# Optimization experiments

Hardware: AMD Instinct MI355X
Metric: run time of the kernel (lower is better)

## Reference

```python
import jax, jax.numpy as jnp
import numpy as np

B, T, P, C = 32, 16, 16, 2048
EPS = 1e-5


def setup_inputs() -> dict:
    key = jax.random.key(0)
    ks = jax.random.split(key, 9)
    s = 0.02
    return {
        "X": jax.random.normal(ks[0], (B, T, P, C), dtype=jnp.float32),
        "W_att": jax.random.normal(ks[1], (C, C), dtype=jnp.float32) * s,
        "b_att": jnp.zeros((C,), dtype=jnp.float32),
        "W1": jax.random.normal(ks[2], (C, C), dtype=jnp.float32) * s,
        "b1": jnp.zeros((C,), dtype=jnp.float32),
        "gamma": jnp.ones((C,), dtype=jnp.float32),
        "beta": jnp.zeros((C,), dtype=jnp.float32),
        "W2": jax.random.normal(ks[3], (C, C), dtype=jnp.float32) * s,
        "b2": jnp.zeros((C,), dtype=jnp.float32),
    }


def reference(X, W_att, b_att, W1, b1, gamma, beta, W2, b2):
    b, t, p, c = X.shape
    Xf = X.reshape(b * t, p, c)                                   # [BT, P, C]
    # per-frame attention gate: mean over parts -> Linear -> sigmoid
    attn = jax.nn.sigmoid(jnp.einsum("nc,dc->nd", Xf.mean(axis=1), W_att) + b_att)
    Xg = Xf * attn[:, None, :]                                    # gate each part
    # gcn: Linear -> per-frame BatchNorm1d (training stats over P) -> ReLU -> Linear
    h = jnp.einsum("npc,dc->npd", Xg, W1) + b1                    # [BT, P, C]
    mu = h.mean(axis=1, keepdims=True)
    var = jnp.mean(jnp.square(h - mu), axis=1, keepdims=True)     # biased var, as torch BN
    hn = (h - mu) * jax.lax.rsqrt(var + EPS) * gamma + beta
    out = jnp.einsum("npc,dc->npd", jax.nn.relu(hn), W2) + b2
    return out.reshape(b, t, p, c)
```

## Files before the change

kernel.cpp:

```cpp
#include <hip/hip_runtime.h>
#include <hip/hip_bf16.h>

typedef __attribute__((ext_vector_type(8))) short short8;
typedef __attribute__((ext_vector_type(4))) float f32x4;

static constexpr int Cdim = 2048;
static constexpr int NFRM = 512;
static constexpr int Pdim = 16;
static constexpr int MROWS = NFRM * Pdim;
static constexpr float EPS = 1e-5f;

__device__ __forceinline__ unsigned short f2b(float x) {
  union { float f; unsigned u; } v; v.f = x;
  unsigned r = v.u + 0x7fffu + ((v.u >> 16) & 1u);
  return (unsigned short)(r >> 16);
}

__device__ __forceinline__ void gload16(const void* g, void* l) {
  __builtin_amdgcn_global_load_lds(
      (const __attribute__((address_space(1))) unsigned int*)g,
      (__attribute__((address_space(3))) unsigned int*)l, 16, 0, 0);
}


__global__ __launch_bounds__(256) void cast3_kernel(
    const float* __restrict__ s0, const float* __restrict__ s1, const float* __restrict__ s2,
    unsigned short* __restrict__ d0, unsigned short* __restrict__ d1, unsigned short* __restrict__ d2)
{
  long i = (long)blockIdx.x * 256 + threadIdx.x;
  const float* s; unsigned short* d; long off;
  if (i < 1048576)      { s = s0; d = d0; off = i; }
  else if (i < 2097152) { s = s1; d = d1; off = i - 1048576; }
  else                  { s = s2; d = d2; off = i - 2097152; }
  float4 v = reinterpret_cast<const float4*>(s)[off];
  union { unsigned short u[4]; unsigned long long q; } o;
  o.u[0] = f2b(v.x); o.u[1] = f2b(v.y); o.u[2] = f2b(v.z); o.u[3] = f2b(v.w);
  *reinterpret_cast<unsigned long long*>(d + off * 4) = o.q;
}

__global__ __launch_bounds__(256) void mean_cast_kernel(
    const float* __restrict__ X, unsigned short* __restrict__ Mb)
{
  int idx = blockIdx.x * 256 + threadIdx.x;
  int n  = idx >> 9;
  int c4 = idx & 511;
  const float4* xp = reinterpret_cast<const float4*>(X) + (long)n * (Pdim * 512) + c4;
  float4 s = {0.f, 0.f, 0.f, 0.f};
  #pragma unroll
  for (int p = 0; p < Pdim; ++p) {
    float4 v = xp[(long)p * 512];
    s.x += v.x; s.y += v.y; s.z += v.z; s.w += v.w;
  }
  const float r = 1.f / 16.f;
  union { unsigned short u[4]; unsigned long long q; } o;
  o.u[0] = f2b(s.x * r); o.u[1] = f2b(s.y * r); o.u[2] = f2b(s.z * r); o.u[3] = f2b(s.w * r);
  *reinterpret_cast<unsigned long long*>(Mb + (long)idx * 4) = o.q;
}

__global__ __launch_bounds__(256) void gate_kernel(
    const float* __restrict__ X, const float* __restrict__ PA, const float* __restrict__ PB,
    const float* __restrict__ b_att, unsigned short* __restrict__ Xg)
{
  constexpr long F = 512L * 2048;
  long idx = (long)blockIdx.x * 256 + threadIdx.x;
  int c4 = (int)(idx & 511);
  long np = idx >> 9;
  long n  = np >> 4;
  float4 x  = reinterpret_cast<const float4*>(X)[idx];
  float4 p0 = reinterpret_cast<const float4*>(PA)[n * 512 + c4];
  float4 p1 = reinterpret_cast<const float4*>(PA + F)[n * 512 + c4];
  float4 p2 = reinterpret_cast<const float4*>(PB)[n * 512 + c4];
  float4 p3 = reinterpret_cast<const float4*>(PB + F)[n * 512 + c4];
  float4 bb = reinterpret_cast<const float4*>(b_att)[c4];
  float4 a;
  a.x = 1.f / (1.f + __expf(-(p0.x + p1.x + p2.x + p3.x + bb.x)));
  a.y = 1.f / (1.f + __expf(-(p0.y + p1.y + p2.y + p3.y + bb.y)));
  a.z = 1.f / (1.f + __expf(-(p0.z + p1.z + p2.z + p3.z + bb.z)));
  a.w = 1.f / (1.f + __expf(-(p0.w + p1.w + p2.w + p3.w + bb.w)));
  union { unsigned short u[4]; unsigned long long q; } o;
  o.u[0] = f2b(x.x * a.x); o.u[1] = f2b(x.y * a.y);
  o.u[2] = f2b(x.z * a.z); o.u[3] = f2b(x.w * a.w);
  *reinterpret_cast<unsigned long long*>(Xg + idx * 4) = o.q;
}

__global__ __launch_bounds__(256) void gemm_att_sk(
    const unsigned short* __restrict__ A,
    const unsigned short* __restrict__ B,
    float* __restrict__ PA, float* __restrict__ PB)
{
  constexpr int N = 2048, K = 2048, KH = 512;
  constexpr long F = 512L * 2048;
  __shared__ unsigned short As[128 * 32];
  __shared__ unsigned short Bs[128 * 32];
  const int t = threadIdx.x;
  const int lane = t & 63;
  const int wid = t >> 6;
  const int wr = wid >> 1, wc = wid & 1;
  const int m0 = blockIdx.x * 128, n0 = blockIdx.y * 128;
  const int k0 = blockIdx.z * KH;
  float* out = (blockIdx.z < 2) ? (PA + (long)blockIdx.z * F) : (PB + (long)(blockIdx.z - 2) * F);

  f32x4 acc[4][4];
  #pragma unroll
  for (int i = 0; i < 4; i++)
    #pragma unroll
    for (int j = 0; j < 4; j++) acc[i][j] = (f32x4){0.f, 0.f, 0.f, 0.f};

  const int srow = t >> 2;
  const int scol = (t & 3) * 8;
  const long aoff0 = (long)(m0 + srow) * K + scol;
  const long aoff1 = (long)(m0 + 64 + srow) * K + scol;
  const long boff0 = (long)(n0 + srow) * K + scol;
  const long boff1 = (long)(n0 + 64 + srow) * K + scol;
  char* AsB = (char*)As;
  char* BsB = (char*)Bs;

  const int fr = lane & 15;
  const int fk = (lane >> 4) * 8;

  for (int kt = k0; kt < k0 + KH; kt += 32) {
    __syncthreads();
    gload16(A + aoff0 + kt, AsB + t * 16);
    gload16(A + aoff1 + kt, AsB + 4096 + t * 16);
    gload16(B + boff0 + kt, BsB + t * 16);
    gload16(B + boff1 + kt, BsB + 4096 + t * 16);
    __syncthreads();
    short8 af[4], bfr[4];
    #pragma unroll
    for (int m = 0; m < 4; m++)
      af[m] = *reinterpret_cast<const short8*>(&As[(wr * 64 + m * 16 + fr) * 32 + fk]);
    #pragma unroll
    for (int n = 0; n < 4; n++)
      bfr[n] = *reinterpret_cast<const short8*>(&Bs[(wc * 64 + n * 16 + fr) * 32 + fk]);
    #pragma unroll
    for (int m = 0; m < 4; m++)
      #pragma unroll
      for (int n = 0; n < 4; n++)
        acc[m][n] = __builtin_amdgcn_mfma_f32_16x16x32_bf16(af[m], bfr[n], acc[m][n], 0, 0, 0);
  }

  const int l4 = lane >> 4;
  #pragma unroll
  for (int m = 0; m < 4; m++) {
    const int r0 = m0 + wr * 64 + m * 16 + l4 * 4;
    #pragma unroll
    for (int n = 0; n < 4; n++) {
      const int cn = n0 + wc * 64 + n * 16 + fr;
      #pragma unroll
      for (int j = 0; j < 4; j++)
        out[(long)(r0 + j) * N + cn] = acc[m][n][j];
    }
  }
}

template<int EPI>
__global__ __launch_bounds__(512, 2) void gemm256(
    const unsigned short* __restrict__ A,
    const unsigned short* __restrict__ Bp,
    int Kk, int Nn, int nbx,
    const float* __restrict__ bias,
    const float* __restrict__ gamma,
    const float* __restrict__ beta,
    float* __restrict__ Cf,
    unsigned short* __restrict__ Cb)
{
  __shared__ char lds[131072];
  const int t = threadIdx.x;
  const int lane = t & 63;
  const int wid = t >> 6;
  const int wr = wid >> 2;
  const int wc = wid & 3;

  const int nw = gridDim.x;
  const int wg = (blockIdx.x & 7) * (nw >> 3) + (blockIdx.x >> 3);
  const int bx = wg % nbx;
  const int by = wg / nbx;
  const int m0 = bx << 8, n0 = by << 8;

  const int NT = Kk >> 6;
  const int NI = NT >> 1;

  const long h64 = (long)64 * Kk, h128 = (long)128 * Kk;
  const int row0 = t >> 3;
  const int col0 = ((t & 7) * 8) ^ ((row0 & 7) << 3);
  const unsigned short* gA = A  + (long)(m0 + row0) * Kk + col0;
  const unsigned short* gB = Bp + (long)(n0 + row0) * Kk + col0;

  const int fr_ = lane & 15;
  const int cb0 = ((lane >> 4) << 4) ^ ((fr_ & 7) << 4);
  const int aB = (wr << 14) + fr_ * 128;
  const int bB = 32768 + ((wc >> 1) << 14) + ((wc & 1) << 13) + fr_ * 128;

#define STG(gp_, ko_, lo_) do { \
    const unsigned short* g0_ = (gp_) + (ko_); \
    gload16(g0_, lds + (lo_) + (t << 4)); \
    gload16(g0_ + h64, lds + (lo_) + 8192 + (t << 4)); } while (0)

#define LDSA(buf_, m_, ks_) (*(const short8*)(lds + (buf_) * 65536 + aB + (m_) * 2048 + (cb0 ^ ((ks_) << 6))))
#define LDSB(buf_, n_, ks_) (*(const short8*)(lds + (buf_) * 65536 + bB + (n_) * 2048 + (cb0 ^ ((ks_) << 6))))

#define RDAF(buf_, mb_) do { \
    af[0][0] = LDSA(buf_, (mb_) + 0, 0); af[0][1] = LDSA(buf_, (mb_) + 0, 1); \
    af[1][0] = LDSA(buf_, (mb_) + 1, 0); af[1][1] = LDSA(buf_, (mb_) + 1, 1); \
    af[2][0] = LDSA(buf_, (mb_) + 2, 0); af[2][1] = LDSA(buf_, (mb_) + 2, 1); \
    af[3][0] = LDSA(buf_, (mb_) + 3, 0); af[3][1] = LDSA(buf_, (mb_) + 3, 1); } while (0)

#define RDB(buf_, nb_, dst_) do { \
    dst_[0][0] = LDSB(buf_, (nb_) + 0, 0); dst_[0][1] = LDSB(buf_, (nb_) + 0, 1); \
    dst_[1][0] = LDSB(buf_, (nb_) + 1, 0); dst_[1][1] = LDSB(buf_, (nb_) + 1, 1); } while (0)

#define QUAD(mb_, nb_, b_) do { \
    _Pragma("unroll") \
    for (int mi = 0; mi < 4; ++mi) { \
      _Pragma("unroll") \
      for (int ni = 0; ni < 2; ++ni) { \
        acc[(mb_) + mi][(nb_) + ni] = __builtin_amdgcn_mfma_f32_16x16x32_bf16(af[mi][0], b_[ni][0], acc[(mb_) + mi][(nb_) + ni], 0, 0, 0); \
        acc[(mb_) + mi][(nb_) + ni] = __builtin_amdgcn_mfma_f32_16x16x32_bf16(af[mi][1], b_[ni][1], acc[(mb_) + mi][(nb_) + ni], 0, 0, 0); \
      } } } while (0)

#define BARX() do { \
    __builtin_amdgcn_sched_barrier(0); \
    __builtin_amdgcn_s_barrier(); \
    __builtin_amdgcn_sched_barrier(0); } while (0)

#define PRIO1() __builtin_amdgcn_s_setprio(1)
#define PRIO0() __builtin_amdgcn_s_setprio(0)
#define VMC(n_) asm volatile("s_waitcnt vmcnt(" #n_ ")" ::: "memory")

  f32x4 acc[8][4];
  #pragma unroll
  for (int i = 0; i < 8; i++)
    #pragma unroll
    for (int j = 0; j < 4; j++) acc[i][j] = (f32x4){0.f, 0.f, 0.f, 0.f};

  short8 af[4][2], b23[2][2], bE0[2][2], bO0[2][2];

  STG(gA, 0, 0);
  STG(gA + h128, 0, 16384);
  STG(gB, 0, 32768);
  STG(gB + h128, 0, 49152);
  STG(gB, 64, 98304);
  STG(gB + h128, 64, 114688);
  VMC(4);
  __builtin_amdgcn_s_barrier();
  __builtin_amdgcn_sched_barrier(0);
  RDB(0, 0, bE0);

#define ITERBODY(LAST_) do { \
     \
    STG(gA, ko + 64, 65536); \
    RDAF(0, 0); \
    BARX(); PRIO1(); QUAD(0, 0, bE0); PRIO0(); \
     \
    STG(gA + h128, ko + 64, 81920); \
    RDB(0, 2, b23); \
    BARX(); PRIO1(); QUAD(0, 2, b23); PRIO0(); \
     \
    VMC(4); \
    if (!(LAST_)) STG(gB, ko + 128, 32768); \
    RDAF(0, 4); \
    BARX(); PRIO1(); QUAD(4, 0, bE0); PRIO0(); \
     \
    if (LAST_) { VMC(0); } else { VMC(2); STG(gB + h128, ko + 128, 49152); } \
    RDB(1, 0, bO0); \
    BARX(); PRIO1(); QUAD(4, 2, b23); PRIO0(); \
     \
    if (!(LAST_)) STG(gA, ko + 128, 0); \
    RDAF(1, 0); \
    BARX(); PRIO1(); QUAD(0, 0, bO0); PRIO0(); \
     \
    if (!(LAST_)) STG(gA + h128, ko + 128, 16384); \
    RDB(1, 2, b23); \
    BARX(); PRIO1(); QUAD(0, 2, b23); PRIO0(); \
     \
    if (!(LAST_)) { VMC(4); STG(gB, ko + 192, 98304); } \
    RDAF(1, 4); \
    BARX(); PRIO1(); QUAD(4, 0, bO0); PRIO0(); \
     \
    if (!(LAST_)) { VMC(2); STG(gB + h128, ko + 192, 114688); RDB(0, 0, bE0); } \
    BARX(); PRIO1(); QUAD(4, 2, b23); PRIO0(); \
  } while (0)

  long ko = 0;
  for (int i = 0; i < NI - 1; ++i, ko += 128) {
    ITERBODY(0);
  }
  ITERBODY(1);

  const int l4 = lane >> 4;
  #pragma unroll
  for (int m = 0; m < 8; ++m) {
    const int r0 = m0 + wr * 128 + m * 16 + l4 * 4;
    #pragma unroll
    for (int n = 0; n < 4; ++n) {
      const int cn = n0 + wc * 64 + n * 16 + fr_;
      if constexpr (EPI == 1) {
        float s1 = 0.f, s2 = 0.f;
        #pragma unroll
        for (int j = 0; j < 4; j++) { float v = acc[m][n][j]; s1 += v; s2 += v * v; }
        s1 += __shfl_xor(s1, 16); s2 += __shfl_xor(s2, 16);
        s1 += __shfl_xor(s1, 32); s2 += __shfl_xor(s2, 32);
        const float mean = s1 * 0.0625f;
        const float var  = s2 * 0.0625f - mean * mean;
        const float sc = rsqrtf(var + EPS) * gamma[cn];
        const float sh = beta[cn] - mean * sc;
        #pragma unroll
        for (int j = 0; j < 4; j++) {
          float v = fmaxf(acc[m][n][j] * sc + sh, 0.f);
          Cb[(long)(r0 + j) * Nn + cn] = f2b(v);
        }
      } else {
        const float bb = bias[cn];
        #pragma unroll
        for (int j = 0; j < 4; j++)
          Cf[(long)(r0 + j) * Nn + cn] = acc[m][n][j] + bb;
      }
    }
  }
#undef STG
#undef LDSA
#undef LDSB
#undef RDAF
#undef RDB
#undef QUAD
#undef BARX
#undef PRIO1
#undef PRIO0
#undef VMC
#undef ITERBODY
}

extern "C" void kernel_launch(void* const* d_in, const int* in_sizes, int n_in,
                              void* d_out, int out_size, void* d_ws, size_t ws_size,
                              hipStream_t stream) {
  const float* X     = (const float*)d_in[0];
  const float* W_att = (const float*)d_in[1];
  const float* b_att = (const float*)d_in[2];
  const float* W1    = (const float*)d_in[3];
  const float* gamma = (const float*)d_in[5];
  const float* beta  = (const float*)d_in[6];
  const float* W2    = (const float*)d_in[7];
  const float* b2    = (const float*)d_in[8];
  float* out = (float*)d_out;

  char* ws = (char*)d_ws;
  unsigned short* Wab = (unsigned short*)(ws + 0);
  unsigned short* W1b = (unsigned short*)(ws + 8388608);
  unsigned short* W2b = (unsigned short*)(ws + 16777216);
  float*          PatA= (float*)        (ws + 25165824);
  unsigned short* Xg  = (unsigned short*)(ws + 33554432);
  unsigned short* Hr  = (unsigned short*)(ws + 67108864);
  unsigned short* Mb  = (unsigned short*)(ws + 67108864);
  float*          PatB= (float*)        (ws + 67108864 + 2097152);

  hipLaunchKernelGGL(cast3_kernel, dim3(12288), dim3(256), 0, stream,
                     W_att, W1, W2, Wab, W1b, W2b);
  hipLaunchKernelGGL(mean_cast_kernel, dim3(1024), dim3(256), 0, stream, X, Mb);
  hipLaunchKernelGGL(gemm_att_sk, dim3(4, 16, 4), dim3(256), 0, stream,
                     Mb, Wab, PatA, PatB);
  hipLaunchKernelGGL(gate_kernel, dim3(16384), dim3(256), 0, stream,
                     X, PatA, PatB, b_att, Xg);
  hipLaunchKernelGGL((gemm256<1>), dim3(256), dim3(512), 0, stream,
                     Xg, W1b, Cdim, Cdim, 32, nullptr, gamma, beta, nullptr, Hr);
  hipLaunchKernelGGL((gemm256<2>), dim3(256), dim3(512), 0, stream,
                     Hr, W2b, Cdim, Cdim, 32, b2, nullptr, nullptr, out, nullptr);
}
```

Baseline: 183.9 us.

## Interleave LDS fragment reads with MFMA groups in GEMM main loop

Reorders the GEMM inner pipeline so the A-fragment LDS reads for the next quad happen inside the current quad's MFMA sequence, using sched_group_barrier hints. B-fragment reads are also moved after the barrier so they overlap with MFMAs instead of sitting before the barrier. The goal is to hide LDS read latency behind matrix-core work. The cost is more live fragment registers, and the reads now depend on barrier placement to stay correct across buffer reuse.

```diff
diff --git a/kernel.cpp b/kernel.cpp
--- a/kernel.cpp
+++ b/kernel.cpp
@@ -209,7 +209,7 @@
     dst_[0][0] = LDSB(buf_, (nb_) + 0, 0); dst_[0][1] = LDSB(buf_, (nb_) + 0, 1); \
     dst_[1][0] = LDSB(buf_, (nb_) + 1, 0); dst_[1][1] = LDSB(buf_, (nb_) + 1, 1); } while (0)
 
-#define QUAD(mb_, nb_, b_) do { \
+#define QUADX(mb_, nb_, b_) do { \
     _Pragma("unroll") \
     for (int mi = 0; mi < 4; ++mi) { \
       _Pragma("unroll") \
@@ -217,6 +217,22 @@
         acc[(mb_) + mi][(nb_) + ni] = __builtin_amdgcn_mfma_f32_16x16x32_bf16(af[mi][0], b_[ni][0], acc[(mb_) + mi][(nb_) + ni], 0, 0, 0); \
         acc[(mb_) + mi][(nb_) + ni] = __builtin_amdgcn_mfma_f32_16x16x32_bf16(af[mi][1], b_[ni][1], acc[(mb_) + mi][(nb_) + ni], 0, 0, 0); \
       } } } while (0)
+
+#define QUAD_RA(mb_, nb_, b_, rbuf_, rmb_, DO_) do { \
+    _Pragma("unroll") \
+    for (int mi = 0; mi < 4; ++mi) { \
+      _Pragma("unroll") \
+      for (int ni = 0; ni < 2; ++ni) { \
+        acc[(mb_) + mi][(nb_) + ni] = __builtin_amdgcn_mfma_f32_16x16x32_bf16(af[mi][0], b_[ni][0], acc[(mb_) + mi][(nb_) + ni], 0, 0, 0); \
+        acc[(mb_) + mi][(nb_) + ni] = __builtin_amdgcn_mfma_f32_16x16x32_bf16(af[mi][1], b_[ni][1], acc[(mb_) + mi][(nb_) + ni], 0, 0, 0); \
+      } \
+      if (DO_) { \
+        af[mi][0] = LDSA(rbuf_, (rmb_) + mi, 0); \
+        af[mi][1] = LDSA(rbuf_, (rmb_) + mi, 1); \
+        __builtin_amdgcn_sched_group_barrier(0x8, 4, 0);    \
+        __builtin_amdgcn_sched_group_barrier(0x100, 2, 0);  \
+      } \
+    } } while (0)
 
 #define BARX() do { \
     __builtin_amdgcn_sched_barrier(0); \
@@ -244,41 +260,55 @@
   VMC(4);
   __builtin_amdgcn_s_barrier();
   __builtin_amdgcn_sched_barrier(0);
+  RDAF(0, 0);
   RDB(0, 0, bE0);
 
 #define ITERBODY(LAST_) do { \
      \
     STG(gA, ko + 64, 65536); \
-    RDAF(0, 0); \
-    BARX(); PRIO1(); QUAD(0, 0, bE0); PRIO0(); \
+    BARX(); PRIO1(); \
+    RDB(0, 2, b23); \
+    QUADX(0, 0, bE0); \
+    PRIO0(); \
      \
     STG(gA + h128, ko + 64, 81920); \
-    RDB(0, 2, b23); \
-    BARX(); PRIO1(); QUAD(0, 2, b23); PRIO0(); \
+    BARX(); PRIO1(); \
+    QUAD_RA(0, 2, b23, 0, 4, 1); \
+    PRIO0(); \
      \
     VMC(4); \
     if (!(LAST_)) STG(gB, ko + 128, 32768); \
-    RDAF(0, 4); \
-    BARX(); PRIO1(); QUAD(4, 0, bE0); PRIO0(); \
+    BARX(); PRIO1(); \
+    RDB(1, 0, bO0); \
+    QUADX(4, 0, bE0); \
+    PRIO0(); \
      \
     if (LAST_) { VMC(0); } else { VMC(2); STG(gB + h128, ko + 128, 49152); } \
-    RDB(1, 0, bO0); \
-    BARX(); PRIO1(); QUAD(4, 2, b23); PRIO0(); \
+    BARX(); PRIO1(); \
+    QUAD_RA(4, 2, b23, 1, 0, 1); \
+    PRIO0(); \
      \
     if (!(LAST_)) STG(gA, ko + 128, 0); \
-    RDAF(1, 0); \
-    BARX(); PRIO1(); QUAD(0, 0, bO0); PRIO0(); \
+    BARX(); PRIO1(); \
+    RDB(1, 2, b23); \
+    QUADX(0, 0, bO0); \
+    PRIO0(); \
      \
     if (!(LAST_)) STG(gA + h128, ko + 128, 16384); \
-    RDB(1, 2, b23); \
-    BARX(); PRIO1(); QUAD(0, 2, b23); PRIO0(); \
+    BARX(); PRIO1(); \
+    QUAD_RA(0, 2, b23, 1, 4, 1); \
+    PRIO0(); \
      \
     if (!(LAST_)) { VMC(4); STG(gB, ko + 192, 98304); } \
-    RDAF(1, 4); \
-    BARX(); PRIO1(); QUAD(4, 0, bO0); PRIO0(); \
-     \
-    if (!(LAST_)) { VMC(2); STG(gB + h128, ko + 192, 114688); RDB(0, 0, bE0); } \
-    BARX(); PRIO1(); QUAD(4, 2, b23); PRIO0(); \
+    BARX(); PRIO1(); \
+    if (!(LAST_)) RDB(0, 0, bE0); \
+    QUADX(4, 0, bO0); \
+    PRIO0(); \
+     \
+    if (!(LAST_)) { VMC(2); STG(gB + h128, ko + 192, 114688); } \
+    BARX(); PRIO1(); \
+    QUAD_RA(4, 2, b23, 0, 0, !(LAST_)); \
+    PRIO0(); \
   } while (0)
 
   long ko = 0;
@@ -322,7 +352,8 @@
 #undef LDSB
 #undef RDAF
 #undef RDB
-#undef QUAD
+#undef QUADX
+#undef QUAD_RA
 #undef BARX
 #undef PRIO1
 #undef PRIO0
```

Measured after the change: 184.7 us. No clear change (+0.4%).

## Restructure GEMM main loop into four barrier phases with interleaved LDS reads

Applied to the files above, without the earlier changes.

The K-loop of the bf16 MFMA GEMM goes from eight barrier-separated quadrant phases to four half-tile phases. All four B fragments are read once per buffer and held for the whole 128-row half, and the A reads for the second half are issued inside the first half's MFMA loop. Global loads are grouped in pairs and the vmcnt waits move to the start of each phase. The aim is fewer s_barriers and more overlap of LDS reads with MFMAs. In exchange, register pressure rises and the correctness of the buffer-reuse ordering is harder to verify.

```diff
diff --git a/kernel.cpp b/kernel.cpp
--- a/kernel.cpp
+++ b/kernel.cpp
@@ -199,30 +199,41 @@
 #define LDSA(buf_, m_, ks_) (*(const short8*)(lds + (buf_) * 65536 + aB + (m_) * 2048 + (cb0 ^ ((ks_) << 6))))
 #define LDSB(buf_, n_, ks_) (*(const short8*)(lds + (buf_) * 65536 + bB + (n_) * 2048 + (cb0 ^ ((ks_) << 6))))
 
-#define RDAF(buf_, mb_) do { \
-    af[0][0] = LDSA(buf_, (mb_) + 0, 0); af[0][1] = LDSA(buf_, (mb_) + 0, 1); \
-    af[1][0] = LDSA(buf_, (mb_) + 1, 0); af[1][1] = LDSA(buf_, (mb_) + 1, 1); \
-    af[2][0] = LDSA(buf_, (mb_) + 2, 0); af[2][1] = LDSA(buf_, (mb_) + 2, 1); \
-    af[3][0] = LDSA(buf_, (mb_) + 3, 0); af[3][1] = LDSA(buf_, (mb_) + 3, 1); } while (0)
-
-#define RDB(buf_, nb_, dst_) do { \
-    dst_[0][0] = LDSB(buf_, (nb_) + 0, 0); dst_[0][1] = LDSB(buf_, (nb_) + 0, 1); \
-    dst_[1][0] = LDSB(buf_, (nb_) + 1, 0); dst_[1][1] = LDSB(buf_, (nb_) + 1, 1); } while (0)
-
-#define QUAD(mb_, nb_, b_) do { \
+#define REGION_RD(buf_) do { \
+    af[0][0] = LDSA(buf_, 0, 0); af[0][1] = LDSA(buf_, 0, 1); \
+    bf0[0][0] = LDSB(buf_, 0, 0); bf0[0][1] = LDSB(buf_, 0, 1); \
+    af[1][0] = LDSA(buf_, 1, 0); af[1][1] = LDSA(buf_, 1, 1); \
+    bf0[1][0] = LDSB(buf_, 1, 0); bf0[1][1] = LDSB(buf_, 1, 1); \
+    af[2][0] = LDSA(buf_, 2, 0); af[2][1] = LDSA(buf_, 2, 1); \
+    b23[0][0] = LDSB(buf_, 2, 0); b23[0][1] = LDSB(buf_, 2, 1); \
+    af[3][0] = LDSA(buf_, 3, 0); af[3][1] = LDSA(buf_, 3, 1); \
+    b23[1][0] = LDSB(buf_, 3, 0); b23[1][1] = LDSB(buf_, 3, 1); } while (0)
+
+#define MF(a_, b_, c_) __builtin_amdgcn_mfma_f32_16x16x32_bf16(a_, b_, c_, 0, 0, 0)
+
+#define MHALF(buf_, base_, EMB_) do { \
     _Pragma("unroll") \
     for (int mi = 0; mi < 4; ++mi) { \
-      _Pragma("unroll") \
-      for (int ni = 0; ni < 2; ++ni) { \
-        acc[(mb_) + mi][(nb_) + ni] = __builtin_amdgcn_mfma_f32_16x16x32_bf16(af[mi][0], b_[ni][0], acc[(mb_) + mi][(nb_) + ni], 0, 0, 0); \
-        acc[(mb_) + mi][(nb_) + ni] = __builtin_amdgcn_mfma_f32_16x16x32_bf16(af[mi][1], b_[ni][1], acc[(mb_) + mi][(nb_) + ni], 0, 0, 0); \
-      } } } while (0)
+      acc[(base_) + mi][0] = MF(af[mi][0], bf0[0][0], acc[(base_) + mi][0]); \
+      acc[(base_) + mi][0] = MF(af[mi][1], bf0[0][1], acc[(base_) + mi][0]); \
+      acc[(base_) + mi][1] = MF(af[mi][0], bf0[1][0], acc[(base_) + mi][1]); \
+      acc[(base_) + mi][1] = MF(af[mi][1], bf0[1][1], acc[(base_) + mi][1]); \
+      acc[(base_) + mi][2] = MF(af[mi][0], b23[0][0], acc[(base_) + mi][2]); \
+      acc[(base_) + mi][2] = MF(af[mi][1], b23[0][1], acc[(base_) + mi][2]); \
+      acc[(base_) + mi][3] = MF(af[mi][0], b23[1][0], acc[(base_) + mi][3]); \
+      acc[(base_) + mi][3] = MF(af[mi][1], b23[1][1], acc[(base_) + mi][3]); \
+      if (EMB_) { af[mi][0] = LDSA(buf_, 4 + mi, 0); af[mi][1] = LDSA(buf_, 4 + mi, 1); } \
+    } } while (0)
 
 #define BARX() do { \
     __builtin_amdgcn_sched_barrier(0); \
     __builtin_amdgcn_s_barrier(); \
     __builtin_amdgcn_sched_barrier(0); } while (0)
 
+#define LGK0() do { \
+    asm volatile("s_waitcnt lgkmcnt(0)" ::: "memory"); \
+    __builtin_amdgcn_sched_barrier(0); } while (0)
+
 #define PRIO1() __builtin_amdgcn_s_setprio(1)
 #define PRIO0() __builtin_amdgcn_s_setprio(0)
 #define VMC(n_) asm volatile("s_waitcnt vmcnt(" #n_ ")" ::: "memory")
@@ -233,7 +244,7 @@
     #pragma unroll
     for (int j = 0; j < 4; j++) acc[i][j] = (f32x4){0.f, 0.f, 0.f, 0.f};
 
-  short8 af[4][2], b23[2][2], bE0[2][2], bO0[2][2];
+  short8 af[4][2], bf0[2][2], b23[2][2];
 
   STG(gA, 0, 0);
   STG(gA + h128, 0, 16384);
@@ -241,44 +252,30 @@
   STG(gB + h128, 0, 49152);
   STG(gB, 64, 98304);
   STG(gB + h128, 64, 114688);
-  VMC(4);
-  __builtin_amdgcn_s_barrier();
-  __builtin_amdgcn_sched_barrier(0);
-  RDB(0, 0, bE0);
 
 #define ITERBODY(LAST_) do { \
      \
+    VMC(4); \
+    BARX(); \
     STG(gA, ko + 64, 65536); \
-    RDAF(0, 0); \
-    BARX(); PRIO1(); QUAD(0, 0, bE0); PRIO0(); \
+    STG(gA + h128, ko + 64, 81920); \
+    REGION_RD(0); \
+    PRIO1(); MHALF(0, 0, 1); PRIO0(); \
+    LGK0(); \
      \
-    STG(gA + h128, ko + 64, 81920); \
-    RDB(0, 2, b23); \
-    BARX(); PRIO1(); QUAD(0, 2, b23); PRIO0(); \
+    BARX(); \
+    if (!(LAST_)) { STG(gA, ko + 128, 0); STG(gA + h128, ko + 128, 16384); } \
+    PRIO1(); MHALF(0, 4, 0); PRIO0(); \
      \
-    VMC(4); \
-    if (!(LAST_)) STG(gB, ko + 128, 32768); \
-    RDAF(0, 4); \
-    BARX(); PRIO1(); QUAD(4, 0, bE0); PRIO0(); \
+    if (LAST_) { VMC(0); } else { VMC(4); } \
+    BARX(); \
+    if (!(LAST_)) { STG(gB, ko + 128, 32768); STG(gB + h128, ko + 128, 49152); } \
+    REGION_RD(1); \
+    PRIO1(); MHALF(1, 0, 1); PRIO0(); \
      \
-    if (LAST_) { VMC(0); } else { VMC(2); STG(gB + h128, ko + 128, 49152); } \
-    RDB(1, 0, bO0); \
-    BARX(); PRIO1(); QUAD(4, 2, b23); PRIO0(); \
-     \
-    if (!(LAST_)) STG(gA, ko + 128, 0); \
-    RDAF(1, 0); \
-    BARX(); PRIO1(); QUAD(0, 0, bO0); PRIO0(); \
-     \
-    if (!(LAST_)) STG(gA + h128, ko + 128, 16384); \
-    RDB(1, 2, b23); \
-    BARX(); PRIO1(); QUAD(0, 2, b23); PRIO0(); \
-     \
-    if (!(LAST_)) { VMC(4); STG(gB, ko + 192, 98304); } \
-    RDAF(1, 4); \
-    BARX(); PRIO1(); QUAD(4, 0, bO0); PRIO0(); \
-     \
-    if (!(LAST_)) { VMC(2); STG(gB + h128, ko + 192, 114688); RDB(0, 0, bE0); } \
-    BARX(); PRIO1(); QUAD(4, 2, b23); PRIO0(); \
+    BARX(); \
+    if (!(LAST_)) { STG(gB, ko + 192, 98304); STG(gB + h128, ko + 192, 114688); } \
+    PRIO1(); MHALF(1, 4, 0); PRIO0(); \
   } while (0)
 
   long ko = 0;
@@ -320,10 +317,11 @@
 #undef STG
 #undef LDSA
 #undef LDSB
-#undef RDAF
-#undef RDB
-#undef QUAD
+#undef REGION_RD
+#undef MF
+#undef MHALF
 #undef BARX
+#undef LGK0
 #undef PRIO1
 #undef PRIO0
 #undef VMC
```

Result: slower. 188.5 us (+2.5%).
